# Kernel tuning notes

Measured on AMD Instinct MI355X. Metric: run time of the kernel, lower is better.

## Reference

```python
import jax, jax.numpy as jnp
import numpy as np

C, H, W = 16, 512, 512
HID = 128
N_STEPS = 8


def setup_inputs() -> dict:
    key = jax.random.key(0)
    k1, k2, k3 = jax.random.split(key, 3)
    state = jax.random.normal(k1, (C, H, W), dtype=jnp.float32)
    # MLP params: 5*C = 80 gathered features -> HID -> C delta channels
    W1 = jax.random.normal(k2, (5 * C, HID), dtype=jnp.float32) * (1.0 / np.sqrt(5 * C))
    b1 = jnp.zeros((HID,), dtype=jnp.float32)
    W2 = jax.random.normal(k3, (HID, C), dtype=jnp.float32) * (1.0 / np.sqrt(HID))
    b2 = jnp.zeros((C,), dtype=jnp.float32)
    return {"state": state, "W1": W1, "b1": b1, "W2": W2, "b2": b2, "n_steps": N_STEPS}


def _neighbor_idx(n):
    i = jnp.arange(n)
    minus = jnp.maximum(i - 1, 0)          # clamp at low edge (cy==0 -> 0)
    plus = jnp.where(i == n - 1, 0, i + 1)  # WRAP to 0 at high edge (original quirk)
    return minus, plus


def reference(state, W1, b1, W2, b2, n_steps):
    c, h, w = state.shape
    up, down = _neighbor_idx(h)
    left, right = _neighbor_idx(w)

    def step(s, _):
        # von-Neumann gather: (5C, H, W), feature order [center, up, down, left, right]
        feats = jnp.concatenate(
            [s, s[:, up, :], s[:, down, :], s[:, :, left], s[:, :, right]], axis=0)
        x = feats.reshape(5 * c, h * w).T        # (HW, 5C)
        hdn = jax.nn.relu(x @ W1 + b1)           # (HW, HID)
        delta = (hdn @ W2 + b2).T.reshape(c, h, w)
        s_new = s + delta
        s_new = s_new.at[0].set(s[0])            # channel 0 snapshot restore
        return s_new, None

    out, _ = jax.lax.scan(step, state, None, length=n_steps)
    return out
```

## Files before the change

kernel.cpp:

```cpp
#include <hip/hip_runtime.h>
#include <hip/hip_bf16.h>

#define HH 512
#define WW 512
#define CC 16
#define HIDN 128
#define HWSZ (HH*WW)

typedef __attribute__((ext_vector_type(8))) short short8;
typedef __attribute__((ext_vector_type(4))) float float4v;

__device__ __forceinline__ short to_bf16(float f){
    __hip_bfloat16 h = __float2bfloat16(f);
    return __builtin_bit_cast(short, h);
}

__global__ void __launch_bounds__(256) prep_kernel(
    const float* __restrict__ W1, const float* __restrict__ W2,
    short* __restrict__ w1t, short* __restrict__ w2t)
{
    int t = blockIdx.x * blockDim.x + threadIdx.x;
    int stride = gridDim.x * blockDim.x;
    for (int idx = t; idx < HIDN*96; idx += stride){
        int n = idx / 96;
        int k = idx - n*96;
        float v = (k < 80) ? W1[k*HIDN + n] : 0.0f;
        w1t[idx] = to_bf16(v);
    }
    for (int idx = t; idx < CC*HIDN; idx += stride){
        int n = idx >> 7;
        int k = idx & 127;
        w2t[idx] = to_bf16(W2[k*CC + n]);
    }
}

__global__ void __launch_bounds__(256) step_kernel(
    const float* __restrict__ src, float* __restrict__ dst,
    const short* __restrict__ w1t, const short* __restrict__ w2t,
    const float* __restrict__ b1, const float* __restrict__ b2)
{
    __shared__ __align__(16) short feats[64][104];
    __shared__ __align__(16) short hdn[64][136];
    __shared__ float sctr[64][17];
    __shared__ float stg[16][65];
    __shared__ float b1s[HIDN];
    __shared__ float b2s[CC];

    const int t    = threadIdx.x;
    const int w    = t >> 6;
    const int lane = t & 63;
    const int ln15 = lane & 15;
    const int g4   = lane >> 4;

    const int bx = blockIdx.x;
    const int y  = bx >> 3;
    const int xs = (bx & 7) << 6;

    if (t < HIDN) b1s[t] = b1[t];
    if (t < CC)   b2s[t] = b2[t];

    const int yu = (y == 0)      ? 0 : (y - 1);
    const int yd = (y == HH - 1) ? 0 : (y + 1);

    {
        const int p  = lane;
        const int x  = xs + p;
        const int xl = (x == 0)      ? 0 : (x - 1);
        const int xr = (x == WW - 1) ? 0 : (x + 1);
        #pragma unroll
        for (int i = 0; i < 3; ++i){
            const int g = w + (i << 2);
            if (g < 10){
                const int n  = g >> 1;
                const int cb = (g & 1) << 3;
                int row, col;
                if      (n == 0){ row = y;  col = x;  }
                else if (n == 1){ row = yu; col = x;  }
                else if (n == 2){ row = yd; col = x;  }
                else if (n == 3){ row = y;  col = xl; }
                else            { row = y;  col = xr; }
                const int base = row * WW + col;
                short8 v;
                #pragma unroll
                for (int j = 0; j < 8; ++j){
                    float f = src[(cb + j) * HWSZ + base];
                    v[j] = to_bf16(f);
                    if (n == 0) sctr[p][cb + j] = f;
                }
                *(short8*)(&feats[p][g << 3]) = v;
            } else {
                short8 z = {0,0,0,0,0,0,0,0};
                *(short8*)(&feats[p][g << 3]) = z;
            }
        }
    }
    __syncthreads();

    float4v acc[4][2];
    #pragma unroll
    for (int mt = 0; mt < 4; ++mt)
        #pragma unroll
        for (int nt = 0; nt < 2; ++nt)
            acc[mt][nt] = (float4v){0.f, 0.f, 0.f, 0.f};

    #pragma unroll
    for (int kk = 0; kk < 3; ++kk){
        const int k0 = kk << 5;
        short8 bfrag[2];
        #pragma unroll
        for (int nt = 0; nt < 2; ++nt){
            const int col = (w << 5) + (nt << 4) + ln15;
            bfrag[nt] = *(const short8*)(w1t + col * 96 + k0 + (g4 << 3));
        }
        #pragma unroll
        for (int mt = 0; mt < 4; ++mt){
            short8 afrag = *(const short8*)(&feats[(mt << 4) + ln15][k0 + (g4 << 3)]);
            #pragma unroll
            for (int nt = 0; nt < 2; ++nt){
                acc[mt][nt] = __builtin_amdgcn_mfma_f32_16x16x32_bf16(
                    afrag, bfrag[nt], acc[mt][nt], 0, 0, 0);
            }
        }
    }

    #pragma unroll
    for (int nt = 0; nt < 2; ++nt){
        const int col  = (w << 5) + (nt << 4) + ln15;
        const float bias = b1s[col];
        #pragma unroll
        for (int mt = 0; mt < 4; ++mt){
            #pragma unroll
            for (int r = 0; r < 4; ++r){
                const int m = (mt << 4) + (g4 << 2) + r;
                float v = acc[mt][nt][r] + bias;
                v = v > 0.f ? v : 0.f;
                hdn[m][col] = to_bf16(v);
            }
        }
    }
    __syncthreads();

    float4v acc2 = (float4v){0.f, 0.f, 0.f, 0.f};
    #pragma unroll
    for (int kk = 0; kk < 4; ++kk){
        const int k0 = kk << 5;
        short8 a = *(const short8*)(&hdn[(w << 4) + ln15][k0 + (g4 << 3)]);
        short8 b = *(const short8*)(w2t + ln15 * HIDN + k0 + (g4 << 3));
        acc2 = __builtin_amdgcn_mfma_f32_16x16x32_bf16(a, b, acc2, 0, 0, 0);
    }

    {
        const int c = ln15;
        const float bias2 = b2s[c];
        #pragma unroll
        for (int r = 0; r < 4; ++r){
            const int p = (w << 4) + (g4 << 2) + r;
            const float sold = sctr[p][c];
            float v = (c == 0) ? sold : (sold + acc2[r] + bias2);
            stg[c][p] = v;
        }
    }
    __syncthreads();

    #pragma unroll
    for (int i = 0; i < 4; ++i){
        const int idx = t + (i << 8);
        const int c2  = idx >> 6;
        const int xo  = idx & 63;
        dst[c2 * HWSZ + y * WW + xs + xo] = stg[c2][xo];
    }
}

extern "C" void kernel_launch(void* const* d_in, const int* in_sizes, int n_in,
                              void* d_out, int out_size, void* d_ws, size_t ws_size,
                              hipStream_t stream)
{
    const float* state = (const float*)d_in[0];
    const float* W1    = (const float*)d_in[1];
    const float* b1    = (const float*)d_in[2];
    const float* W2    = (const float*)d_in[3];
    const float* b2    = (const float*)d_in[4];

    float* B1  = (float*)d_ws;
    short* w1t = (short*)((char*)d_ws + (size_t)HWSZ * CC * 4);
    short* w2t = w1t + HIDN * 96;
    float* out = (float*)d_out;

    prep_kernel<<<32, 256, 0, stream>>>(W1, W2, w1t, w2t);

    dim3 grid(HH * (WW / 64));
    step_kernel<<<grid, 256, 0, stream>>>(state, B1, w1t, w2t, b1, b2);
    step_kernel<<<grid, 256, 0, stream>>>(B1, out, w1t, w2t, b1, b2);
    step_kernel<<<grid, 256, 0, stream>>>(out, B1, w1t, w2t, b1, b2);
    step_kernel<<<grid, 256, 0, stream>>>(B1, out, w1t, w2t, b1, b2);
    step_kernel<<<grid, 256, 0, stream>>>(out, B1, w1t, w2t, b1, b2);
    step_kernel<<<grid, 256, 0, stream>>>(B1, out, w1t, w2t, b1, b2);
    step_kernel<<<grid, 256, 0, stream>>>(out, B1, w1t, w2t, b1, b2);
    step_kernel<<<grid, 256, 0, stream>>>(B1, out, w1t, w2t, b1, b2);
}
```

Measured before the change: 309.3 us.

## Stage three bf16 halo rows in LDS and build stencil MFMA fragments from offsets

Replaces the per-thread scalar gather of five neighbor features (80 strided float loads per pixel group) with float4 vector loads of the center, up and down rows into a bf16 shared-memory row buffer. Left and right halo pixels are loaded separately. A-fragments for the first GEMM are then read from shifted offsets in that buffer instead of a materialized 5C feature tile. The padded K slots now hold duplicate data rather than zeros, which relies on the zero-padded W1 rows. The staging buffer is reused for the output transpose, and an occupancy hint of 5 blocks per SM is added through launch bounds.

```diff
diff --git a/kernel.cpp b/kernel.cpp
--- a/kernel.cpp
+++ b/kernel.cpp
@@ -8,6 +8,7 @@
 #define HWSZ (HH*WW)
 
 typedef __attribute__((ext_vector_type(8))) short short8;
+typedef __attribute__((ext_vector_type(4))) short short4v;
 typedef __attribute__((ext_vector_type(4))) float float4v;
 
 __device__ __forceinline__ short to_bf16(float f){
@@ -34,17 +35,21 @@
     }
 }
 
-__global__ void __launch_bounds__(256) step_kernel(
+#define RSTRIDE 24
+#define RROW    (68*RSTRIDE)
+
+__global__ void __launch_bounds__(256, 5) step_kernel(
     const float* __restrict__ src, float* __restrict__ dst,
     const short* __restrict__ w1t, const short* __restrict__ w2t,
     const float* __restrict__ b1, const float* __restrict__ b2)
 {
-    __shared__ __align__(16) short feats[64][104];
+    __shared__ __align__(16) short rows_u[3*RROW];
     __shared__ __align__(16) short hdn[64][136];
-    __shared__ float sctr[64][17];
-    __shared__ float stg[16][65];
+    __shared__ __align__(16) float sctr[64][16];
     __shared__ float b1s[HIDN];
     __shared__ float b2s[CC];
+
+    float (*stg)[65] = (float (*)[65])rows_u;
 
     const int t    = threadIdx.x;
     const int w    = t >> 6;
@@ -62,39 +67,48 @@
     const int yu = (y == 0)      ? 0 : (y - 1);
     const int yd = (y == HH - 1) ? 0 : (y + 1);
 
-    {
-        const int p  = lane;
-        const int x  = xs + p;
-        const int xl = (x == 0)      ? 0 : (x - 1);
-        const int xr = (x == WW - 1) ? 0 : (x + 1);
-        #pragma unroll
-        for (int i = 0; i < 3; ++i){
-            const int g = w + (i << 2);
-            if (g < 10){
-                const int n  = g >> 1;
-                const int cb = (g & 1) << 3;
-                int row, col;
-                if      (n == 0){ row = y;  col = x;  }
-                else if (n == 1){ row = yu; col = x;  }
-                else if (n == 2){ row = yd; col = x;  }
-                else if (n == 3){ row = y;  col = xl; }
-                else            { row = y;  col = xr; }
-                const int base = row * WW + col;
-                short8 v;
-                #pragma unroll
-                for (int j = 0; j < 8; ++j){
-                    float f = src[(cb + j) * HWSZ + base];
-                    v[j] = to_bf16(f);
-                    if (n == 0) sctr[p][cb + j] = f;
-                }
-                *(short8*)(&feats[p][g << 3]) = v;
-            } else {
-                short8 z = {0,0,0,0,0,0,0,0};
-                *(short8*)(&feats[p][g << 3]) = z;
+    if (t < 192){
+        const int r  = t >> 6;
+        const int l  = t & 63;
+        const int q  = l & 15;
+        const int cq = l >> 4;
+        const int rowg = (r == 0) ? y : ((r == 1) ? yu : yd);
+        const float* base = src + (size_t)rowg * WW + xs + (q << 2);
+        float4v f[4];
+        #pragma unroll
+        for (int i = 0; i < 4; ++i)
+            f[i] = *(const float4v*)(base + (size_t)((cq << 2) + i) * HWSZ);
+        #pragma unroll
+        for (int j = 0; j < 4; ++j){
+            short4v v;
+            v[0] = to_bf16(f[0][j]); v[1] = to_bf16(f[1][j]);
+            v[2] = to_bf16(f[2][j]); v[3] = to_bf16(f[3][j]);
+            *(short4v*)&rows_u[r*RROW + ((q << 2) + 1 + j)*RSTRIDE + (cq << 2)] = v;
+            if (r == 0){
+                float4v g = {f[0][j], f[1][j], f[2][j], f[3][j]};
+                *(float4v*)&sctr[(q << 2) + j][cq << 2] = g;
             }
         }
+    } else if (t < 224){
+        const int c    = (t - 192) & 15;
+        const int side = (t - 192) >> 4;
+        const int gx   = (side == 0) ? ((xs == 0) ? 0 : xs - 1)
+                                     : ((xs + 64 == WW) ? 0 : xs + 64);
+        rows_u[(side * 65)*RSTRIDE + c] =
+            to_bf16(src[(size_t)c*HWSZ + (size_t)y*WW + gx]);
     }
     __syncthreads();
+
+    int offA[3];
+    #pragma unroll
+    for (int kk = 0; kk < 3; ++kk){
+        const int g  = (kk < 2) ? ((kk << 2) + g4) : (8 + (g4 & 1));
+        const int n  = g >> 1;
+        const int cb = (g & 1) << 3;
+        const int r  = (n == 1) ? 1 : ((n == 2) ? 2 : 0);
+        const int dx = (n == 3) ? -1 : ((n == 4) ? 1 : 0);
+        offA[kk] = r*RROW + (ln15 + 1 + dx)*RSTRIDE + cb;
+    }
 
     float4v acc[4][2];
     #pragma unroll
@@ -105,16 +119,15 @@
 
     #pragma unroll
     for (int kk = 0; kk < 3; ++kk){
-        const int k0 = kk << 5;
         short8 bfrag[2];
         #pragma unroll
         for (int nt = 0; nt < 2; ++nt){
             const int col = (w << 5) + (nt << 4) + ln15;
-            bfrag[nt] = *(const short8*)(w1t + col * 96 + k0 + (g4 << 3));
+            bfrag[nt] = *(const short8*)(w1t + col * 96 + (kk << 5) + (g4 << 3));
         }
         #pragma unroll
         for (int mt = 0; mt < 4; ++mt){
-            short8 afrag = *(const short8*)(&feats[(mt << 4) + ln15][k0 + (g4 << 3)]);
+            short8 afrag = *(const short8*)(&rows_u[offA[kk] + mt * (16 * RSTRIDE)]);
             #pragma unroll
             for (int nt = 0; nt < 2; ++nt){
                 acc[mt][nt] = __builtin_amdgcn_mfma_f32_16x16x32_bf16(
@@ -167,7 +180,7 @@
         const int idx = t + (i << 8);
         const int c2  = idx >> 6;
         const int xo  = idx & 63;
-        dst[c2 * HWSZ + y * WW + xs + xo] = stg[c2][xo];
+        dst[(size_t)c2 * HWSZ + (size_t)y * WW + xs + xo] = stg[c2][xo];
     }
 }
 
```

Measured after the change: 262.6 us. 15.1% less time.
